# Optimization experiments

Measured on AMD Instinct MI355X. Metric: run time of the kernel, lower is better.

The kernel has to match this reference:

```python
import jax, jax.numpy as jnp
import numpy as np

B = 1024          # batch
N = 48            # NUM_NOTES
OCT = 12          # OCTAVE
NOCT = 4          # NUM_OCTAVES
TU = 256          # TIME_AXIS_UNITS
NU = 128          # NOTE_AXIS_UNITS
IN_T = 1 + OCT + (2 * OCT + 1) + OCT  # 50, time-axis LSTM input
IN_N = TU + 1                          # 257, note-axis LSTM input


def setup_inputs() -> dict:
    key = jax.random.key(0)
    ks = jax.random.split(key, 16)
    s = 0.05
    w = lambda k, shape: jax.random.normal(k, shape, jnp.float32) * s
    return dict(
        note_input=(jax.random.uniform(ks[0], (B, N)) < 0.1).astype(jnp.float32),
        targets=(jax.random.uniform(ks[1], (B, N)) < 0.1).astype(jnp.float32),
        # TimeAxis 2-layer LSTM (b = b_ih + b_hh fused, mathematically identical)
        t_Wih0=w(ks[2], (4 * TU, IN_T)), t_Whh0=w(ks[3], (4 * TU, TU)), t_b0=w(ks[4], (4 * TU,)),
        t_Wih1=w(ks[5], (4 * TU, TU)), t_Whh1=w(ks[6], (4 * TU, TU)), t_b1=w(ks[7], (4 * TU,)),
        # NoteAxis 2-layer LSTM
        n_Wih0=w(ks[8], (4 * NU, IN_N)), n_Whh0=w(ks[9], (4 * NU, NU)), n_b0=w(ks[10], (4 * NU,)),
        n_Wih1=w(ks[11], (4 * NU, NU)), n_Whh1=w(ks[12], (4 * NU, NU)), n_b1=w(ks[13], (4 * NU,)),
        out_W=w(ks[14], (1, NU)), out_b=w(ks[15], (1,)),
    )


def lstm_cell(x, h, c, Wih, Whh, b):
    # PyTorch LSTM gate order: i, f, g, o
    g = x @ Wih.T + h @ Whh.T + b
    i, f, gg, o = jnp.split(g, 4, axis=-1)
    c = jax.nn.sigmoid(f) * c + jax.nn.sigmoid(i) * jnp.tanh(gg)
    h = jax.nn.sigmoid(o) * jnp.tanh(c)
    return h, c


def reference(note_input, targets,
              t_Wih0, t_Whh0, t_b0, t_Wih1, t_Whh1, t_b1,
              n_Wih0, n_Whh0, n_b0, n_Wih1, n_Whh1, n_b1,
              out_W, out_b):
    # ---- TimeAxis (states=None => every note is an independent single LSTM step) ----
    pitch_pos = jnp.arange(N, dtype=jnp.float32) / N                      # [N]
    pitch_class = jnp.tile(jnp.eye(OCT, dtype=jnp.float32), (NOCT, 1))    # [N, OCT]
    chord = note_input.reshape(B, OCT, NOCT).sum(-1)                      # [B, OCT]
    xp = jnp.pad(note_input, ((0, 0), (OCT, OCT)))                        # [B, N+2*OCT]
    vic_idx = jnp.arange(N)[:, None] + jnp.arange(2 * OCT + 1)[None, :]   # [N, 25]
    vicinity = xp[:, vic_idx]                                             # [B, N, 25]
    rnn_in = jnp.concatenate([
        jnp.broadcast_to(pitch_pos[None, :, None], (B, N, 1)),
        jnp.broadcast_to(pitch_class[None], (B, N, OCT)),
        vicinity,
        jnp.broadcast_to(chord[:, None, :], (B, N, OCT)),
    ], axis=-1).reshape(B * N, IN_T)
    z = jnp.zeros((B * N, TU), rnn_in.dtype)
    h1, _ = lstm_cell(rnn_in, z, z, t_Wih0, t_Whh0, t_b0)
    h2, _ = lstm_cell(h1, z, z, t_Wih1, t_Whh1, t_b1)
    feats = h2.reshape(B, N, TU)                                          # [B, N, TU]

    # ---- NoteAxis (teacher-forced sequential LSTM over notes) ----
    cond = jnp.concatenate([jnp.zeros((B, 1), feats.dtype), targets[:, :-1]], axis=1)  # [B, N]
    xs = jnp.concatenate([feats, cond[..., None]], axis=-1).transpose(1, 0, 2)  # [N, B, IN_N]
    z1 = jnp.zeros((B, NU), feats.dtype)

    def step(carry, x):
        h1, c1, h2, c2 = carry
        h1, c1 = lstm_cell(x, h1, c1, n_Wih0, n_Whh0, n_b0)
        h2, c2 = lstm_cell(h1, h2, c2, n_Wih1, n_Whh1, n_b1)
        return (h1, c1, h2, c2), h2

    _, hs = jax.lax.scan(step, (z1, z1, z1, z1), xs)                      # [N, B, NU]
    out = jax.nn.sigmoid(jnp.einsum('nbh,oh->bno', hs, out_W) + out_b)    # [B, N, 1]
    return out[..., 0]
```

## Files before the change

### kernel.cpp

```cpp
#include <hip/hip_runtime.h>

typedef unsigned short ushort_t;
typedef unsigned int uint_t;
typedef _Float16 f16_t;
typedef _Float16 half8_t __attribute__((ext_vector_type(8)));
typedef float floatx4 __attribute__((ext_vector_type(4)));
typedef unsigned int uintx4 __attribute__((ext_vector_type(4)));

__device__ __forceinline__ ushort_t f2h_bits(float f) {
    f16_t h = (f16_t)f;
    return __builtin_bit_cast(ushort_t, h);
}
__device__ __forceinline__ float h2f(ushort_t u) {
    return (float)__builtin_bit_cast(f16_t, u);
}
__device__ __forceinline__ float h2f_lo(uint_t u) { return h2f((ushort_t)(u & 0xFFFF)); }
__device__ __forceinline__ float h2f_hi(uint_t u) { return h2f((ushort_t)(u >> 16)); }
__device__ __forceinline__ float sigm(float x) {
    return __builtin_amdgcn_rcpf(1.0f + __expf(-x));
}
__device__ __forceinline__ float tanhx(float x) {
    return __builtin_fmaf(-2.0f, __builtin_amdgcn_rcpf(1.0f + __expf(2.0f * x)), 1.0f);
}
__device__ __forceinline__ half8_t h8(uint4 v) { return __builtin_bit_cast(half8_t, v); }

__device__ __forceinline__ half8_t ldfrag(const ushort_t* p, int V, int kt, int q, int n) {
    return *(const half8_t*)(p + ((size_t)((kt * 4 + q) * V + n)) * 8);
}

__device__ __forceinline__ void pack_one(
    const float* srcA, int KA, const float* srcB, int KB,
    ushort_t* dst, int V, int K, int idx)
{
    int v = idx / K, k = idx - v * K;
    float val = 0.0f;
    if (k < KA) val = srcA[v * KA + k];
    else if (k < KA + KB) val = srcB[v * KB + (k - KA)];
    int kt = k >> 5, qq = (k >> 3) & 3, j = k & 7;
    dst[((size_t)((kt * 4 + qq) * V + v)) * 8 + j] = f2h_bits(val);
}

__device__ __forceinline__ void pack_tl_one(
    const float* src, int Ksrc, ushort_t* dst, int K, int idx)
{
    int v = idx / K, k = idx - v * K;
    int r = (v < 256) ? v : v + 256;
    float val = (k < Ksrc) ? src[r * Ksrc + k] : 0.0f;
    int kt = k >> 5, qq = (k >> 3) & 3, j = k & 7;
    dst[((size_t)((kt * 4 + qq) * 768 + v)) * 8 + j] = f2h_bits(val);
}

__global__ __launch_bounds__(256) void packAll(
    const float* __restrict__ tWih0, const float* __restrict__ tWih1,
    const float* __restrict__ nWih0, const float* __restrict__ nWhh0,
    const float* __restrict__ nWih1, const float* __restrict__ nWhh1,
    ushort_t* __restrict__ W0m, ushort_t* __restrict__ W1m,
    ushort_t* __restrict__ N0x, ushort_t* __restrict__ N0m,
    ushort_t* __restrict__ N1m)
{
    int idx = blockIdx.x * 256 + threadIdx.x;
    if (idx < 49152) { pack_tl_one(tWih0, 50, W0m, 64, idx); return; }
    idx -= 49152;
    if (idx < 196608) { pack_tl_one(tWih1, 256, W1m, 256, idx); return; }
    idx -= 196608;
    if (idx < 131072) { pack_one(nWih0, 257, (const float*)0, 0, N0x, 512, 256, idx); return; }
    idx -= 131072;
    if (idx < 65536) { pack_one(nWhh0, 128, (const float*)0, 0, N0m, 512, 128, idx); return; }
    idx -= 65536;
    if (idx < 131072) { pack_one(nWih1, 128, nWhh1, 128, N1m, 512, 256, idx); return; }
}

__global__ __launch_bounds__(512, 6) void fusedA(
    const float* __restrict__ note, const float* __restrict__ targets,
    const ushort_t* __restrict__ W0m, const float* __restrict__ b0,
    const ushort_t* __restrict__ W1m, const float* __restrict__ b1,
    const ushort_t* __restrict__ N0x, const float* __restrict__ nWih0raw,
    const float* __restrict__ nb0,
    uint_t* __restrict__ G1u)
{
    __shared__ __align__(16) ushort_t xAa[32 * 64];
    __shared__ __align__(16) ushort_t xH1[32 * 256];
    __shared__ __align__(16) ushort_t xH2[32 * 256];
    const int tid = threadIdx.x;
    const int wv = tid >> 6, l = tid & 63, l16 = l & 15, q = l >> 4;
    const int r0A = blockIdx.x * 32;

    for (int idx = tid; idx < 32 * 64; idx += 512) {
        int r = idx >> 6, c = idx & 63;
        int row = r0A + r;
        int b = row / 48, n = row - b * 48;
        float val = 0.0f;
        if (c == 0) val = (float)n * (1.0f / 48.0f);
        else if (c < 13) val = ((n % 12) == (c - 1)) ? 1.0f : 0.0f;
        else if (c < 38) {
            int p = n + (c - 13) - 12;
            if (p >= 0 && p < 48) val = note[b * 48 + p];
        } else if (c < 50) {
            const float* nb = note + b * 48 + (c - 38) * 4;
            val = nb[0] + nb[1] + nb[2] + nb[3];
        }
        int kb = c >> 3, j = c & 7;
        xAa[r * 64 + (((kb ^ r) & 7) << 3) + j] = f2h_bits(val);
    }
    __syncthreads();

#pragma unroll
    for (int s = 0; s < 2; ++s) {
        const int u = (wv * 2 + s) * 16 + l16;
        floatx4 acc[2][3] = {};
#pragma unroll
        for (int kt = 0; kt < 2; ++kt) {
            half8_t bI = ldfrag(W0m, 768, kt, q, u);
            half8_t bG = ldfrag(W0m, 768, kt, q, 256 + u);
            half8_t bO = ldfrag(W0m, 768, kt, q, 512 + u);
            int kbp = ((kt * 4 + q) ^ l16) & 7;
#pragma unroll
            for (int mt = 0; mt < 2; ++mt) {
                half8_t a = *(const half8_t*)&xAa[(mt * 16 + l16) * 64 + kbp * 8];
                acc[mt][0] = __builtin_amdgcn_mfma_f32_16x16x32_f16(a, bI, acc[mt][0], 0, 0, 0);
                acc[mt][1] = __builtin_amdgcn_mfma_f32_16x16x32_f16(a, bG, acc[mt][1], 0, 0, 0);
                acc[mt][2] = __builtin_amdgcn_mfma_f32_16x16x32_f16(a, bO, acc[mt][2], 0, 0, 0);
            }
        }
        float bi = b0[u], bg = b0[512 + u], bo = b0[768 + u];
        int kbW = u >> 3;
#pragma unroll
        for (int mt = 0; mt < 2; ++mt)
#pragma unroll
            for (int r = 0; r < 4; ++r) {
                float c = sigm(acc[mt][0][r] + bi) * tanhx(acc[mt][1][r] + bg);
                float h = sigm(acc[mt][2][r] + bo) * tanhx(c);
                int m = mt * 16 + q * 4 + r;
                int kbp = (kbW & 16) | ((kbW ^ (m & 15)) & 15);
                xH1[m * 256 + kbp * 8 + (u & 7)] = f2h_bits(h);
            }
    }
    __syncthreads();

#pragma unroll
    for (int s = 0; s < 2; ++s) {
        const int u = (wv * 2 + s) * 16 + l16;
        floatx4 acc[2][3] = {};
#pragma unroll
        for (int kt = 0; kt < 8; ++kt) {
            half8_t bI = ldfrag(W1m, 768, kt, q, u);
            half8_t bG = ldfrag(W1m, 768, kt, q, 256 + u);
            half8_t bO = ldfrag(W1m, 768, kt, q, 512 + u);
            int kb = kt * 4 + q;
            int kbp = (kb & 16) | ((kb ^ l16) & 15);
#pragma unroll
            for (int mt = 0; mt < 2; ++mt) {
                half8_t a = *(const half8_t*)&xH1[(mt * 16 + l16) * 256 + kbp * 8];
                acc[mt][0] = __builtin_amdgcn_mfma_f32_16x16x32_f16(a, bI, acc[mt][0], 0, 0, 0);
                acc[mt][1] = __builtin_amdgcn_mfma_f32_16x16x32_f16(a, bG, acc[mt][1], 0, 0, 0);
                acc[mt][2] = __builtin_amdgcn_mfma_f32_16x16x32_f16(a, bO, acc[mt][2], 0, 0, 0);
            }
        }
        float bi = b1[u], bg = b1[512 + u], bo = b1[768 + u];
        int kbW = u >> 3;
#pragma unroll
        for (int mt = 0; mt < 2; ++mt)
#pragma unroll
            for (int r = 0; r < 4; ++r) {
                float c = sigm(acc[mt][0][r] + bi) * tanhx(acc[mt][1][r] + bg);
                float h = sigm(acc[mt][2][r] + bo) * tanhx(c);
                int m = mt * 16 + q * 4 + r;
                int kbp = (kbW & 16) | ((kbW ^ (m & 15)) & 15);
                xH2[m * 256 + kbp * 8 + (u & 7)] = f2h_bits(h);
            }
    }
    __syncthreads();

    {
        const int u2 = wv * 16 + l16;
        floatx4 acc[2][4] = {};
#pragma unroll
        for (int kt = 0; kt < 8; ++kt) {
            half8_t bf[4];
#pragma unroll
            for (int g = 0; g < 4; ++g) bf[g] = ldfrag(N0x, 512, kt, q, g * 128 + u2);
            int kb = kt * 4 + q;
            int kbp = (kb & 16) | ((kb ^ l16) & 15);
#pragma unroll
            for (int mt = 0; mt < 2; ++mt) {
                half8_t a = *(const half8_t*)&xH2[(mt * 16 + l16) * 256 + kbp * 8];
#pragma unroll
                for (int g = 0; g < 4; ++g)
                    acc[mt][g] = __builtin_amdgcn_mfma_f32_16x16x32_f16(a, bf[g], acc[mt][g], 0, 0, 0);
            }
        }
        float bias[4], wc[4];
#pragma unroll
        for (int g = 0; g < 4; ++g) {
            bias[g] = nb0[g * 128 + u2];
            wc[g] = nWih0raw[(size_t)(g * 128 + u2) * 257 + 256];
        }
#pragma unroll
        for (int mt = 0; mt < 2; ++mt) {
#pragma unroll
            for (int r = 0; r < 4; ++r) {
                int R = r0A + mt * 16 + q * 4 + r;
                int b = R / 48;
                int t = R - b * 48;
                float cond = (t > 0) ? targets[R - 1] : 0.0f;
                float vi = acc[mt][0][r] + bias[0] + cond * wc[0];
                float vf = acc[mt][1][r] + bias[1] + cond * wc[1];
                float vg = acc[mt][2][r] + bias[2] + cond * wc[2];
                float vo = acc[mt][3][r] + bias[3] + cond * wc[3];
                uint_t lo = (uint_t)f2h_bits(vi) | ((uint_t)f2h_bits(vf) << 16);
                uint_t hi = (uint_t)f2h_bits(vg) | ((uint_t)f2h_bits(vo) << 16);
                size_t a = ((size_t)(b >> 4) * 48 + t) * 4096 + (b & 15) * 256 + u2 * 2;
                *(uint2*)(G1u + a) = make_uint2(lo, hi);
            }
        }
    }
}

__global__ __launch_bounds__(512) __attribute__((amdgpu_waves_per_eu(2, 2)))
void phaseB(
    const uint_t* __restrict__ G1u, const ushort_t* __restrict__ N0m,
    const ushort_t* __restrict__ N1m, const float* __restrict__ nb1,
    const float* __restrict__ outW, const float* __restrict__ outb,
    float* __restrict__ out)
{
    __shared__ __align__(16) ushort_t w1s[16 * 512 * 8];
    __shared__ __align__(16) ushort_t xA[16 * 512];
    __shared__ __align__(16) float ghead[2][8][16];
    const int tid = threadIdx.x;
    const int wv = tid >> 6, l = tid & 63, l16 = l & 15, q = l >> 4;
    const int r0 = blockIdx.x * 16;
    const int u = wv * 16 + l16;

    for (int i = tid; i < 8192; i += 512) ((uint4*)w1s)[i] = ((const uint4*)N0m)[i];
    for (int i = tid; i < 1024; i += 512) ((uint4*)xA)[i] = make_uint4(0, 0, 0, 0);

    uintx4 B2[8][4];
#pragma unroll
    for (int kt = 0; kt < 8; ++kt)
#pragma unroll
        for (int g = 0; g < 4; ++g)
            B2[kt][g] = *(const uintx4*)(N1m + ((size_t)((kt * 4 + q) * 512 + g * 128 + u)) * 8);

    const float bI = nb1[u], bF = nb1[128 + u], bG = nb1[256 + u], bO = nb1[384 + u];
    const float ob = outb[0];
    const float owf = outW[u];
    float c1[4], c2[4] = {0, 0, 0, 0};

    const uint_t* g1base = G1u + (size_t)blockIdx.x * 48 * 4096;
    uint2 gp0[4], g1c[4], g1n[4];
#pragma unroll
    for (int r = 0; r < 4; ++r)
        gp0[r] = *(const uint2*)(g1base + (q * 4 + r) * 256 + u * 2);
#pragma unroll
    for (int r = 0; r < 4; ++r)
        g1c[r] = *(const uint2*)(g1base + 4096 + (q * 4 + r) * 256 + u * 2);

    const int kbW = u >> 3;
    const int jW = u & 7;

    __syncthreads();

#pragma unroll
    for (int r = 0; r < 4; ++r) {
        float gi = h2f_lo(gp0[r].x);
        float gg = h2f_lo(gp0[r].y);
        float go = h2f_hi(gp0[r].y);
        c1[r] = sigm(gi) * tanhx(gg);
        float h1v = sigm(go) * tanhx(c1[r]);
        int m = q * 4 + r;
        xA[m * 512 + (((kbW ^ m) & 15) << 3) + jW] = f2h_bits(h1v);
    }
    __syncthreads();

    for (int t = 0; t < 48; ++t) {
#pragma unroll
        for (int kt = 0; kt < 8; ++kt)
#pragma unroll
            for (int g = 0; g < 4; ++g)
                asm volatile("" : "+v"(B2[kt][g]));

        if (t > 0 && tid < 16) {
            float s = 0.0f;
#pragma unroll
            for (int w = 0; w < 8; ++w) s += ghead[(t - 1) & 1][w][tid];
            out[(r0 + tid) * 48 + (t - 1)] = sigm(s + ob);
        }

        {
            int tn = (t < 46) ? t + 2 : 47;
            const uint_t* gp = g1base + (size_t)tn * 4096;
#pragma unroll
            for (int r = 0; r < 4; ++r)
                g1n[r] = *(const uint2*)(gp + (q * 4 + r) * 256 + u * 2);
        }

        const int c = (t & 1) * 128;
        const int pv = c ^ 128;

        half8_t a1[4], a2[4];
#pragma unroll
        for (int kt = 0; kt < 4; ++kt) {
            int kb = kt * 4 + q;
            int kbp = (kb ^ l16) & 15;
            a1[kt] = *(const half8_t*)&xA[l16 * 512 + c + kbp * 8];
            a2[kt] = *(const half8_t*)&xA[l16 * 512 + 256 + pv + kbp * 8];
        }

        floatx4 acc1[4] = {};
#pragma unroll
        for (int kt = 0; kt < 4; ++kt) {
            int kb = kt * 4 + q;
#pragma unroll
            for (int g = 0; g < 4; ++g) {
                half8_t bfr = *(const half8_t*)&w1s[((size_t)(kb * 512 + g * 128 + u)) * 8];
                acc1[g] = __builtin_amdgcn_mfma_f32_16x16x32_f16(a1[kt], bfr, acc1[g], 0, 0, 0);
            }
        }

        floatx4 acc2[4] = {};
#pragma unroll
        for (int kt = 0; kt < 4; ++kt)
#pragma unroll
            for (int g = 0; g < 4; ++g)
                acc2[g] = __builtin_amdgcn_mfma_f32_16x16x32_f16(
                    a2[kt], __builtin_bit_cast(half8_t, B2[kt + 4][g]), acc2[g], 0, 0, 0);
#pragma unroll
        for (int kt = 0; kt < 4; ++kt)
#pragma unroll
            for (int g = 0; g < 4; ++g)
                acc2[g] = __builtin_amdgcn_mfma_f32_16x16x32_f16(
                    a1[kt], __builtin_bit_cast(half8_t, B2[kt][g]), acc2[g], 0, 0, 0);

        float p[4];
#pragma unroll
        for (int r = 0; r < 4; ++r) {
            float gi = acc2[0][r] + bI;
            float gf = acc2[1][r] + bF;
            float gg = acc2[2][r] + bG;
            float go = acc2[3][r] + bO;
            c2[r] = sigm(gf) * c2[r] + sigm(gi) * tanhx(gg);
            float h2v = sigm(go) * tanhx(c2[r]);
            int m = q * 4 + r;
            xA[m * 512 + 256 + c + (((kbW ^ m) & 15) << 3) + jW] = f2h_bits(h2v);
            p[r] = h2v * owf;
        }
#pragma unroll
        for (int mask = 1; mask < 16; mask <<= 1)
#pragma unroll
            for (int r = 0; r < 4; ++r) p[r] += __shfl_xor(p[r], mask, 64);
        if (l16 == 0) {
#pragma unroll
            for (int r = 0; r < 4; ++r) ghead[t & 1][wv][q * 4 + r] = p[r];
        }

        if (t < 47) {
#pragma unroll
            for (int r = 0; r < 4; ++r) {
                float gi = acc1[0][r] + h2f_lo(g1c[r].x);
                float gf = acc1[1][r] + h2f_hi(g1c[r].x);
                float gg = acc1[2][r] + h2f_lo(g1c[r].y);
                float go = acc1[3][r] + h2f_hi(g1c[r].y);
                c1[r] = sigm(gf) * c1[r] + sigm(gi) * tanhx(gg);
                float h1v = sigm(go) * tanhx(c1[r]);
                int m = q * 4 + r;
                xA[m * 512 + pv + (((kbW ^ m) & 15) << 3) + jW] = f2h_bits(h1v);
            }
        }
#pragma unroll
        for (int r = 0; r < 4; ++r) g1c[r] = g1n[r];
        __syncthreads();
    }

    if (tid < 16) {
        float s = 0.0f;
#pragma unroll
        for (int w = 0; w < 8; ++w) s += ghead[1][w][tid];
        out[(r0 + tid) * 48 + 47] = sigm(s + ob);
    }
}

extern "C" void kernel_launch(void* const* d_in, const int* in_sizes, int n_in,
                              void* d_out, int out_size, void* d_ws, size_t ws_size,
                              hipStream_t stream)
{
    const float* note  = (const float*)d_in[0];
    const float* targ  = (const float*)d_in[1];
    const float* tWih0 = (const float*)d_in[2];
    const float* tb0   = (const float*)d_in[4];
    const float* tWih1 = (const float*)d_in[5];
    const float* tb1   = (const float*)d_in[7];
    const float* nWih0 = (const float*)d_in[8];
    const float* nWhh0 = (const float*)d_in[9];
    const float* nb0   = (const float*)d_in[10];
    const float* nWih1 = (const float*)d_in[11];
    const float* nWhh1 = (const float*)d_in[12];
    const float* nb1   = (const float*)d_in[13];
    const float* outW  = (const float*)d_in[14];
    const float* outb  = (const float*)d_in[15];

    char* ws = (char*)d_ws;
    uint_t*   G1u = (uint_t*)(ws);
    ushort_t* W0m = (ushort_t*)(ws + 50331648);
    ushort_t* W1m = (ushort_t*)(ws + 50429952);
    ushort_t* N0x = (ushort_t*)(ws + 50823168);
    ushort_t* N0m = (ushort_t*)(ws + 51085312);
    ushort_t* N1m = (ushort_t*)(ws + 51216384);

    packAll<<<2240, 256, 0, stream>>>(tWih0, tWih1, nWih0, nWhh0, nWih1, nWhh1,
                                      W0m, W1m, N0x, N0m, N1m);
    fusedA<<<1536, 512, 0, stream>>>(note, targ, W0m, tb0, W1m, tb1, N0x, nWih0, nb0, G1u);
    phaseB<<<64, 512, 0, stream>>>(G1u, N0m, N1m, nb1, outW, outb, (float*)d_out);
}
```

Baseline: 290.3 us.

## Prescale gate weights by log2e and compute output head with MFMA

New measurement: 269.6 us. -7.1%, faster.

```diff
diff --git a/kernel.cpp b/kernel.cpp
--- a/kernel.cpp
+++ b/kernel.cpp
@@ -7,6 +7,9 @@
 typedef float floatx4 __attribute__((ext_vector_type(4)));
 typedef unsigned int uintx4 __attribute__((ext_vector_type(4)));
 
+#define LOG2E 1.44269504088896f
+#define TWO_LOG2E 2.88539008177793f
+
 __device__ __forceinline__ ushort_t f2h_bits(float f) {
     f16_t h = (f16_t)f;
     return __builtin_bit_cast(ushort_t, h);
@@ -16,13 +19,16 @@
 }
 __device__ __forceinline__ float h2f_lo(uint_t u) { return h2f((ushort_t)(u & 0xFFFF)); }
 __device__ __forceinline__ float h2f_hi(uint_t u) { return h2f((ushort_t)(u >> 16)); }
-__device__ __forceinline__ float sigm(float x) {
-    return __builtin_amdgcn_rcpf(1.0f + __expf(-x));
-}
-__device__ __forceinline__ float tanhx(float x) {
-    return __builtin_fmaf(-2.0f, __builtin_amdgcn_rcpf(1.0f + __expf(2.0f * x)), 1.0f);
-}
-__device__ __forceinline__ half8_t h8(uint4 v) { return __builtin_bit_cast(half8_t, v); }
+
+__device__ __forceinline__ float sigm2(float x) {
+    return __builtin_amdgcn_rcpf(1.0f + __builtin_amdgcn_exp2f(-x));
+}
+__device__ __forceinline__ float tanh2(float y) {
+    return __builtin_fmaf(-2.0f, __builtin_amdgcn_rcpf(1.0f + __builtin_amdgcn_exp2f(y)), 1.0f);
+}
+__device__ __forceinline__ float tanhc(float c) {
+    return tanh2(c * TWO_LOG2E);
+}
 
 __device__ __forceinline__ half8_t ldfrag(const ushort_t* p, int V, int kt, int q, int n) {
     return *(const half8_t*)(p + ((size_t)((kt * 4 + q) * V + n)) * 8);
@@ -36,8 +42,9 @@
     float val = 0.0f;
     if (k < KA) val = srcA[v * KA + k];
     else if (k < KA + KB) val = srcB[v * KB + (k - KA)];
+    float sc = ((v >> 7) == 2) ? TWO_LOG2E : LOG2E;
     int kt = k >> 5, qq = (k >> 3) & 3, j = k & 7;
-    dst[((size_t)((kt * 4 + qq) * V + v)) * 8 + j] = f2h_bits(val);
+    dst[((size_t)((kt * 4 + qq) * V + v)) * 8 + j] = f2h_bits(val * sc);
 }
 
 __device__ __forceinline__ void pack_tl_one(
@@ -46,8 +53,9 @@
     int v = idx / K, k = idx - v * K;
     int r = (v < 256) ? v : v + 256;
     float val = (k < Ksrc) ? src[r * Ksrc + k] : 0.0f;
+    float sc = (v >= 256 && v < 512) ? TWO_LOG2E : LOG2E;
     int kt = k >> 5, qq = (k >> 3) & 3, j = k & 7;
-    dst[((size_t)((kt * 4 + qq) * 768 + v)) * 8 + j] = f2h_bits(val);
+    dst[((size_t)((kt * 4 + qq) * 768 + v)) * 8 + j] = f2h_bits(val * sc);
 }
 
 __global__ __launch_bounds__(256) void packAll(
@@ -122,14 +130,14 @@
                 acc[mt][2] = __builtin_amdgcn_mfma_f32_16x16x32_f16(a, bO, acc[mt][2], 0, 0, 0);
             }
         }
-        float bi = b0[u], bg = b0[512 + u], bo = b0[768 + u];
+        float bi = b0[u] * LOG2E, bg = b0[512 + u] * TWO_LOG2E, bo = b0[768 + u] * LOG2E;
         int kbW = u >> 3;
 #pragma unroll
         for (int mt = 0; mt < 2; ++mt)
 #pragma unroll
             for (int r = 0; r < 4; ++r) {
-                float c = sigm(acc[mt][0][r] + bi) * tanhx(acc[mt][1][r] + bg);
-                float h = sigm(acc[mt][2][r] + bo) * tanhx(c);
+                float c = sigm2(acc[mt][0][r] + bi) * tanh2(acc[mt][1][r] + bg);
+                float h = sigm2(acc[mt][2][r] + bo) * tanhc(c);
                 int m = mt * 16 + q * 4 + r;
                 int kbp = (kbW & 16) | ((kbW ^ (m & 15)) & 15);
                 xH1[m * 256 + kbp * 8 + (u & 7)] = f2h_bits(h);
@@ -156,14 +164,14 @@
                 acc[mt][2] = __builtin_amdgcn_mfma_f32_16x16x32_f16(a, bO, acc[mt][2], 0, 0, 0);
             }
         }
-        float bi = b1[u], bg = b1[512 + u], bo = b1[768 + u];
+        float bi = b1[u] * LOG2E, bg = b1[512 + u] * TWO_LOG2E, bo = b1[768 + u] * LOG2E;
         int kbW = u >> 3;
 #pragma unroll
         for (int mt = 0; mt < 2; ++mt)
 #pragma unroll
             for (int r = 0; r < 4; ++r) {
-                float c = sigm(acc[mt][0][r] + bi) * tanhx(acc[mt][1][r] + bg);
-                float h = sigm(acc[mt][2][r] + bo) * tanhx(c);
+                float c = sigm2(acc[mt][0][r] + bi) * tanh2(acc[mt][1][r] + bg);
+                float h = sigm2(acc[mt][2][r] + bo) * tanhc(c);
                 int m = mt * 16 + q * 4 + r;
                 int kbp = (kbW & 16) | ((kbW ^ (m & 15)) & 15);
                 xH2[m * 256 + kbp * 8 + (u & 7)] = f2h_bits(h);
@@ -192,8 +200,9 @@
         float bias[4], wc[4];
 #pragma unroll
         for (int g = 0; g < 4; ++g) {
-            bias[g] = nb0[g * 128 + u2];
-            wc[g] = nWih0raw[(size_t)(g * 128 + u2) * 257 + 256];
+            float sc = (g == 2) ? TWO_LOG2E : LOG2E;
+            bias[g] = nb0[g * 128 + u2] * sc;
+            wc[g] = nWih0raw[(size_t)(g * 128 + u2) * 257 + 256] * sc;
         }
 #pragma unroll
         for (int mt = 0; mt < 2; ++mt) {
@@ -225,7 +234,7 @@
 {
     __shared__ __align__(16) ushort_t w1s[16 * 512 * 8];
     __shared__ __align__(16) ushort_t xA[16 * 512];
-    __shared__ __align__(16) float ghead[2][8][16];
+    __shared__ __align__(16) ushort_t owfs[128];
     const int tid = threadIdx.x;
     const int wv = tid >> 6, l = tid & 63, l16 = l & 15, q = l >> 4;
     const int r0 = blockIdx.x * 16;
@@ -233,6 +242,12 @@
 
     for (int i = tid; i < 8192; i += 512) ((uint4*)w1s)[i] = ((const uint4*)N0m)[i];
     for (int i = tid; i < 1024; i += 512) ((uint4*)xA)[i] = make_uint4(0, 0, 0, 0);
+    if (tid < 16) {
+        int base = (tid >> 2) * 32 + (tid & 3) * 8;
+#pragma unroll
+        for (int j = 0; j < 8; ++j)
+            owfs[tid * 8 + j] = f2h_bits(outW[base + j] * LOG2E);
+    }
 
     uintx4 B2[8][4];
 #pragma unroll
@@ -241,35 +256,35 @@
         for (int g = 0; g < 4; ++g)
             B2[kt][g] = *(const uintx4*)(N1m + ((size_t)((kt * 4 + q) * 512 + g * 128 + u)) * 8);
 
-    const float bI = nb1[u], bF = nb1[128 + u], bG = nb1[256 + u], bO = nb1[384 + u];
-    const float ob = outb[0];
-    const float owf = outW[u];
+    const float bI = nb1[u] * LOG2E, bF = nb1[128 + u] * LOG2E;
+    const float bG = nb1[256 + u] * TWO_LOG2E, bO = nb1[384 + u] * LOG2E;
+    const float obs = outb[0] * LOG2E;
     float c1[4], c2[4] = {0, 0, 0, 0};
 
     const uint_t* g1base = G1u + (size_t)blockIdx.x * 48 * 4096;
-    uint2 gp0[4], g1c[4], g1n[4];
+    uint2 g1c[4];
 #pragma unroll
     for (int r = 0; r < 4; ++r)
-        gp0[r] = *(const uint2*)(g1base + (q * 4 + r) * 256 + u * 2);
+        g1c[r] = *(const uint2*)(g1base + (q * 4 + r) * 256 + u * 2);
+
+    const int kbW = u >> 3;
+    const int jW = u & 7;
+
+    __syncthreads();
+
+#pragma unroll
+    for (int r = 0; r < 4; ++r) {
+        float gi = h2f_lo(g1c[r].x);
+        float gg = h2f_lo(g1c[r].y);
+        float go = h2f_hi(g1c[r].y);
+        c1[r] = sigm2(gi) * tanh2(gg);
+        float h1v = sigm2(go) * tanhc(c1[r]);
+        int m = q * 4 + r;
+        xA[m * 512 + (((kbW ^ m) & 15) << 3) + jW] = f2h_bits(h1v);
+    }
 #pragma unroll
     for (int r = 0; r < 4; ++r)
         g1c[r] = *(const uint2*)(g1base + 4096 + (q * 4 + r) * 256 + u * 2);
-
-    const int kbW = u >> 3;
-    const int jW = u & 7;
-
-    __syncthreads();
-
-#pragma unroll
-    for (int r = 0; r < 4; ++r) {
-        float gi = h2f_lo(gp0[r].x);
-        float gg = h2f_lo(gp0[r].y);
-        float go = h2f_hi(gp0[r].y);
-        c1[r] = sigm(gi) * tanhx(gg);
-        float h1v = sigm(go) * tanhx(c1[r]);
-        int m = q * 4 + r;
-        xA[m * 512 + (((kbW ^ m) & 15) << 3) + jW] = f2h_bits(h1v);
-    }
     __syncthreads();
 
     for (int t = 0; t < 48; ++t) {
@@ -278,21 +293,6 @@
 #pragma unroll
             for (int g = 0; g < 4; ++g)
                 asm volatile("" : "+v"(B2[kt][g]));
-
-        if (t > 0 && tid < 16) {
-            float s = 0.0f;
-#pragma unroll
-            for (int w = 0; w < 8; ++w) s += ghead[(t - 1) & 1][w][tid];
-            out[(r0 + tid) * 48 + (t - 1)] = sigm(s + ob);
-        }
-
-        {
-            int tn = (t < 46) ? t + 2 : 47;
-            const uint_t* gp = g1base + (size_t)tn * 4096;
-#pragma unroll
-            for (int r = 0; r < 4; ++r)
-                g1n[r] = *(const uint2*)(gp + (q * 4 + r) * 256 + u * 2);
-        }
 
         const int c = (t & 1) * 128;
         const int pv = c ^ 128;
@@ -318,12 +318,16 @@
         }
 
         floatx4 acc2[4] = {};
-#pragma unroll
-        for (int kt = 0; kt < 4; ++kt)
+        floatx4 accH = {0.0f, 0.0f, 0.0f, 0.0f};
+#pragma unroll
+        for (int kt = 0; kt < 4; ++kt) {
 #pragma unroll
             for (int g = 0; g < 4; ++g)
                 acc2[g] = __builtin_amdgcn_mfma_f32_16x16x32_f16(
                     a2[kt], __builtin_bit_cast(half8_t, B2[kt + 4][g]), acc2[g], 0, 0, 0);
+            half8_t of = *(const half8_t*)&owfs[(kt * 4 + q) * 8];
+            accH = __builtin_amdgcn_mfma_f32_16x16x32_f16(a2[kt], of, accH, 0, 0, 0);
+        }
 #pragma unroll
         for (int kt = 0; kt < 4; ++kt)
 #pragma unroll
@@ -331,26 +335,22 @@
                 acc2[g] = __builtin_amdgcn_mfma_f32_16x16x32_f16(
                     a1[kt], __builtin_bit_cast(half8_t, B2[kt][g]), acc2[g], 0, 0, 0);
 
-        float p[4];
+        if (t > 0 && wv == 0 && l16 == 0) {
+#pragma unroll
+            for (int r = 0; r < 4; ++r)
+                out[(r0 + q * 4 + r) * 48 + (t - 1)] = sigm2(accH[r] + obs);
+        }
+
 #pragma unroll
         for (int r = 0; r < 4; ++r) {
             float gi = acc2[0][r] + bI;
             float gf = acc2[1][r] + bF;
             float gg = acc2[2][r] + bG;
             float go = acc2[3][r] + bO;
-            c2[r] = sigm(gf) * c2[r] + sigm(gi) * tanhx(gg);
-            float h2v = sigm(go) * tanhx(c2[r]);
+            c2[r] = sigm2(gf) * c2[r] + sigm2(gi) * tanh2(gg);
+            float h2v = sigm2(go) * tanhc(c2[r]);
             int m = q * 4 + r;
             xA[m * 512 + 256 + c + (((kbW ^ m) & 15) << 3) + jW] = f2h_bits(h2v);
-            p[r] = h2v * owf;
-        }
-#pragma unroll
-        for (int mask = 1; mask < 16; mask <<= 1)
-#pragma unroll
-            for (int r = 0; r < 4; ++r) p[r] += __shfl_xor(p[r], mask, 64);
-        if (l16 == 0) {
-#pragma unroll
-            for (int r = 0; r < 4; ++r) ghead[t & 1][wv][q * 4 + r] = p[r];
         }
 
         if (t < 47) {
@@ -360,22 +360,38 @@
                 float gf = acc1[1][r] + h2f_hi(g1c[r].x);
                 float gg = acc1[2][r] + h2f_lo(g1c[r].y);
                 float go = acc1[3][r] + h2f_hi(g1c[r].y);
-                c1[r] = sigm(gf) * c1[r] + sigm(gi) * tanhx(gg);
-                float h1v = sigm(go) * tanhx(c1[r]);
+                c1[r] = sigm2(gf) * c1[r] + sigm2(gi) * tanh2(gg);
+                float h1v = sigm2(go) * tanhc(c1[r]);
                 int m = q * 4 + r;
                 xA[m * 512 + pv + (((kbW ^ m) & 15) << 3) + jW] = f2h_bits(h1v);
             }
         }
-#pragma unroll
-        for (int r = 0; r < 4; ++r) g1c[r] = g1n[r];
+
+        {
+            int tn = (t < 46) ? t + 2 : 47;
+            const uint_t* gp = g1base + (size_t)tn * 4096;
+#pragma unroll
+            for (int r = 0; r < 4; ++r)
+                g1c[r] = *(const uint2*)(gp + (q * 4 + r) * 256 + u * 2);
+        }
         __syncthreads();
     }
 
-    if (tid < 16) {
-        float s = 0.0f;
-#pragma unroll
-        for (int w = 0; w < 8; ++w) s += ghead[1][w][tid];
-        out[(r0 + tid) * 48 + 47] = sigm(s + ob);
+    {
+        floatx4 accH = {0.0f, 0.0f, 0.0f, 0.0f};
+#pragma unroll
+        for (int kt = 0; kt < 4; ++kt) {
+            int kb = kt * 4 + q;
+            int kbp = (kb ^ l16) & 15;
+            half8_t a2e = *(const half8_t*)&xA[l16 * 512 + 256 + 128 + kbp * 8];
+            half8_t of = *(const half8_t*)&owfs[(kt * 4 + q) * 8];
+            accH = __builtin_amdgcn_mfma_f32_16x16x32_f16(a2e, of, accH, 0, 0, 0);
+        }
+        if (wv == 0 && l16 == 0) {
+#pragma unroll
+            for (int r = 0; r < 4; ++r)
+                out[(r0 + q * 4 + r) * 48 + 47] = sigm2(accH[r] + obs);
+        }
     }
 }
 
```
